# Optimization experiments

Measured on AMD Instinct MI355X. Metric: run time of the kernel, lower is better.

## Reference

```python
import jax, jax.numpy as jnp
import numpy as np

N_ENV = 100000
D_PS = 512
N_SPECIES = 4
N_SUPPORT = 256
N_STRUCT = 1000
ZETA = 2


def setup_inputs() -> dict:
    key = jax.random.key(0)
    k1, k2, k3, k4, k5 = jax.random.split(key, 5)
    power_spectrum = jax.random.normal(k1, (N_ENV, D_PS), dtype=jnp.float32)
    sp = jax.random.normal(k2, (N_SPECIES, N_SUPPORT, D_PS), dtype=jnp.float32)
    # CosineKernel asserts support points are unit-norm
    support_points = sp / jnp.linalg.norm(sp, axis=-1, keepdims=True)
    weights = jax.random.normal(k3, (N_SPECIES, 1, N_SUPPORT), dtype=jnp.float32)
    all_species = jax.random.randint(k4, (N_ENV,), 0, N_SPECIES, dtype=jnp.int64)
    structure_ids = jnp.sort(jax.random.randint(k5, (N_ENV,), 0, N_STRUCT, dtype=jnp.int64))
    return {
        "power_spectrum": power_spectrum,
        "support_points": support_points,
        "weights": weights,
        "all_species": all_species,
        "structure_ids": structure_ids,
    }


def reference(power_spectrum, support_points, weights, all_species, structure_ids):
    # Normalize each environment's power spectrum (CosineKernel)
    ps = power_spectrum / jnp.linalg.norm(power_spectrum, axis=1, keepdims=True)
    # Kernel of every environment against every species' support set: [N, S, M]
    k = jnp.einsum("nd,smd->nsm", ps, support_points) ** ZETA
    # Per-row energy contribution for each species: k @ weights[s].T -> [N, S]
    contrib = jnp.einsum("nsm,sm->ns", k, weights[:, 0, :])
    # Species masking: each row only contributes through its own species' kernel
    onehot = jax.nn.one_hot(all_species, N_SPECIES, dtype=contrib.dtype)  # [N, S]
    per_row = jnp.sum(contrib * onehot, axis=1)  # [N]
    # Segmented sum over structures (equivalent to looping over structures_slices)
    energy = jax.ops.segment_sum(per_row, structure_ids, num_segments=N_STRUCT)
    return energy[:, None]  # [n_structures, 1]
```

## Files before the change

kernel.cpp:

```cpp
#include <hip/hip_runtime.h>
#include <hip/hip_bf16.h>


constexpr int kNEnv     = 100000;
constexpr int kDPS      = 512;
constexpr int kNSpecies = 4;
constexpr int kNSupport = 256;
constexpr int kCap      = 32768;

constexpr int BN = 64;
constexpr int BK = 32;

typedef __attribute__((ext_vector_type(8))) short short8;
typedef __attribute__((ext_vector_type(4))) float f32x4;

__device__ __forceinline__ short8 pack_bf16x8(const float4& a, const float4& b) {
  union { short8 v; __hip_bfloat162 h[4]; } u;
  u.h[0] = __float22bfloat162_rn({a.x, a.y});
  u.h[1] = __float22bfloat162_rn({a.z, a.w});
  u.h[2] = __float22bfloat162_rn({b.x, b.y});
  u.h[3] = __float22bfloat162_rn({b.z, b.w});
  return u.v;
}

__global__ void scatter_convert_kernel(const float* __restrict__ sp,
                                       const int* __restrict__ species,
                                       const int* __restrict__ sid,
                                       int* __restrict__ cnt, int* __restrict__ perm,
                                       int* __restrict__ sidp, short* __restrict__ spb) {
  const int t = threadIdx.x;
  const int b = blockIdx.x;
  if (b < (kNSpecies * kNSupport * kDPS) / (256 * 8)) {
    const int base = (b * 256 + t) * 8;
    const float4 lo = *(const float4*)(sp + base);
    const float4 hi = *(const float4*)(sp + base + 4);
    *(short8*)(spb + base) = pack_bf16x8(lo, hi);
  }
  const int wv   = t >> 6;
  const int lane = t & 63;
  const int i    = b * 256 + t;
  const bool v   = i < kNEnv;
  int s = -1, g = 0;
  if (v) { s = species[i]; g = sid[i]; }

  unsigned long long m[kNSpecies];
  #pragma unroll
  for (int k = 0; k < kNSpecies; ++k) m[k] = __ballot(s == k);
  int r = 0;
  if (v) r = __popcll(m[s] & ((1ull << lane) - 1ull));

  __shared__ int wcnt[4][kNSpecies];
  __shared__ int wbase[4][kNSpecies];
  if (lane < kNSpecies) wcnt[wv][lane] = (int)__popcll(m[lane]);
  __syncthreads();
  if (t < kNSpecies) {
    const int k = t;
    const int tot = wcnt[0][k] + wcnt[1][k] + wcnt[2][k] + wcnt[3][k];
    int p = tot ? atomicAdd(&cnt[k], tot) : 0;
    #pragma unroll
    for (int wvi = 0; wvi < 4; ++wvi) { wbase[wvi][k] = p; p += wcnt[wvi][k]; }
  }
  __syncthreads();
  if (v) {
    const int d = s * kCap + wbase[wv][s] + r;
    perm[d] = i;
    sidp[d] = g;
  }
}

__global__ __launch_bounds__(256, 3) void gap_gemm_v8(
    const float* __restrict__ ps, const short* __restrict__ spb,
    const float* __restrict__ w, const int* __restrict__ cnt,
    const int* __restrict__ perm, const int* __restrict__ sidp,
    float* __restrict__ energy) {
  const int s     = blockIdx.z;
  const int count = min(cnt[s], kCap);
  const int tile0 = blockIdx.x * BN;
  if (tile0 >= count) return;

  __shared__ short a_lds[4][BN][32];
  __shared__ float red[4][BN];
  __shared__ float sqs[BN];

  const int tid  = threadIdx.x;
  const int wv   = tid >> 6;
  const int lane = tid & 63;
  const int l15  = lane & 15;
  const int lq   = lane >> 4;

  const int r0 = wv * 16 + (lane >> 2);
  const int q  = lane & 3;
  int ge = tile0 + r0;
  ge = ge < count ? ge : count - 1;
  const float* asrc = ps + (size_t)perm[s * kCap + ge] * kDPS + q * 8;

  const short* bptr[4];
  float wgt[4];
  const float* w_s = w + s * kNSupport;
  #pragma unroll
  for (int fj = 0; fj < 4; ++fj) {
    const int m = wv * 64 + fj * 16 + l15;
    bptr[fj] = spb + ((size_t)s * kNSupport + m) * kDPS + lq * 8;
    wgt[fj]  = w_s[m];
  }

  f32x4 acc[4][4];
  #pragma unroll
  for (int fi = 0; fi < 4; ++fi)
    #pragma unroll
    for (int fj = 0; fj < 4; ++fj) acc[fi][fj] = (f32x4)0.f;
  float sq = 0.f;

  float4 R[8];
  short8 bf0[4], bf1[4];

#define GLOAD8(G) do {                                                    \
    _Pragma("unroll")                                                     \
    for (int u = 0; u < 8; ++u)                                           \
      R[u] = *(const float4*)(asrc + (G) * 128 + (u >> 1) * 32 + (u & 1) * 4); \
  } while (0)

#define AWRITE8() do {                                                    \
    _Pragma("unroll")                                                     \
    for (int j = 0; j < 4; ++j) {                                         \
      const float4 va = R[2 * j], vb = R[2 * j + 1];                      \
      sq += va.x * va.x + va.y * va.y + va.z * va.z + va.w * va.w         \
          + vb.x * vb.x + vb.y * vb.y + vb.z * vb.z + vb.w * vb.w;        \
      *(short8*)&a_lds[j][r0][q * 8] = pack_bf16x8(va, vb);               \
    }                                                                     \
  } while (0)

#define BLOAD8(T, BF) do {                                                \
    _Pragma("unroll")                                                     \
    for (int fj = 0; fj < 4; ++fj)                                        \
      BF[fj] = *(const short8*)(bptr[fj] + (T) * BK);                     \
  } while (0)

#define ASTEP8(J, BF) do {                                                \
    short8 af[4];                                                         \
    _Pragma("unroll")                                                     \
    for (int fi = 0; fi < 4; ++fi)                                        \
      af[fi] = *(const short8*)&a_lds[J][fi * 16 + l15][lq * 8];          \
    __builtin_amdgcn_s_setprio(1);                                        \
    _Pragma("unroll")                                                     \
    for (int fi = 0; fi < 4; ++fi)                                        \
      _Pragma("unroll")                                                   \
      for (int fj = 0; fj < 4; ++fj)                                      \
        acc[fi][fj] = __builtin_amdgcn_mfma_f32_16x16x32_bf16(            \
            af[fi], BF[fj], acc[fi][fj], 0, 0, 0);                        \
    __builtin_amdgcn_s_setprio(0);                                        \
  } while (0)

#define GROUP8(G) do {                                                    \
    __builtin_amdgcn_s_barrier();              \
    AWRITE8();                                                            \
    asm volatile("s_waitcnt lgkmcnt(0)" ::: "memory");                    \
    __builtin_amdgcn_s_barrier();                     \
    __builtin_amdgcn_sched_barrier(0);                                    \
    if ((G) < 3) GLOAD8((G) + 1);             \
    __builtin_amdgcn_sched_barrier(0);                                    \
    BLOAD8((G) * 4 + 1, bf1); ASTEP8(0, bf0);                             \
    BLOAD8((G) * 4 + 2, bf0); ASTEP8(1, bf1);                             \
    BLOAD8((G) * 4 + 3, bf1); ASTEP8(2, bf0);                             \
    if ((G) < 3) BLOAD8((G) * 4 + 4, bf0);                                \
    ASTEP8(3, bf1);                                                       \
  } while (0)

  GLOAD8(0);
  BLOAD8(0, bf0);
  GROUP8(0);
  GROUP8(1);
  GROUP8(2);
  GROUP8(3);

#undef GROUP8
#undef ASTEP8
#undef BLOAD8
#undef AWRITE8
#undef GLOAD8

  sq += __shfl_xor(sq, 1, 64);
  sq += __shfl_xor(sq, 2, 64);
  if (q == 0) sqs[r0] = sq;

  #pragma unroll
  for (int fi = 0; fi < 4; ++fi) {
    #pragma unroll
    for (int r = 0; r < 4; ++r) {
      float p = 0.f;
      #pragma unroll
      for (int fj = 0; fj < 4; ++fj) {
        const float c = acc[fi][fj][r];
        p += c * c * wgt[fj];
      }
      p += __shfl_xor(p, 1, 64);
      p += __shfl_xor(p, 2, 64);
      p += __shfl_xor(p, 4, 64);
      p += __shfl_xor(p, 8, 64);
      if (l15 == 0) red[wv][fi * 16 + lq * 4 + r] = p;
    }
  }
  __syncthreads();
  if (tid < BN) {
    const float v = red[0][tid] + red[1][tid] + red[2][tid] + red[3][tid];
    const int g  = tile0 + tid;
    if (g < count) atomicAdd(&energy[sidp[s * kCap + g]], v / sqs[tid]);
  }
}

extern "C" void kernel_launch(void* const* d_in, const int* in_sizes, int n_in,
                              void* d_out, int out_size, void* d_ws, size_t ws_size,
                              hipStream_t stream) {
  const float* ps      = (const float*)d_in[0];
  const float* sp      = (const float*)d_in[1];
  const float* w       = (const float*)d_in[2];
  const int*   species = (const int*)d_in[3];
  const int*   sid     = (const int*)d_in[4];
  float* energy = (float*)d_out;

  char* wsb = (char*)d_ws;
  constexpr size_t kOffPerm = 256;
  constexpr size_t kOffSidp = kOffPerm + (size_t)kNSpecies * kCap * 4;
  constexpr size_t kOffSpb  = kOffSidp + (size_t)kNSpecies * kCap * 4;

  int*   cnt  = (int*)wsb;
  int*   perm = (int*)(wsb + kOffPerm);
  int*   sidp = (int*)(wsb + kOffSidp);
  short* spb  = (short*)(wsb + kOffSpb);

  hipMemsetAsync(cnt, 0, 16, stream);
  hipMemsetAsync(energy, 0, out_size * sizeof(float), stream);

  scatter_convert_kernel<<<(kNEnv + 255) / 256, 256, 0, stream>>>(
      sp, species, sid, cnt, perm, sidp, spb);

  dim3 grid(kCap / BN, 1, kNSpecies);
  gap_gemm_v8<<<grid, 256, 0, stream>>>(ps, spb, w, cnt, perm, sidp, energy);
}
```

Before: 337.6 us.

## Pre-tile bf16 support points for coalesced B loads and widen A-row gathers

The conversion kernel now writes the bf16 support points in a fragment-tiled layout, so each wave's MFMA B operand for a k-step is one contiguous 512-element block and the loads coalesce. The A gather is reorganised so each half-wave reads one full 512-byte contiguous row chunk, with per-row squared norms kept in eight partial sums and reduced by shuffles. All 16 B fragments for a group are loaded up front instead of being double-buffered per step. The launch-bounds occupancy hint of 3 is dropped. Holding 16 B fragments raises register pressure and may lower occupancy.

```diff
diff --git a/kernel.cpp b/kernel.cpp
--- a/kernel.cpp
+++ b/kernel.cpp
@@ -9,9 +9,9 @@
 constexpr int kCap      = 32768;
 
 constexpr int BN = 64;
-constexpr int BK = 32;
 
 typedef __attribute__((ext_vector_type(8))) short short8;
+typedef __attribute__((ext_vector_type(4))) short short4v;
 typedef __attribute__((ext_vector_type(4))) float f32x4;
 
 __device__ __forceinline__ short8 pack_bf16x8(const float4& a, const float4& b) {
@@ -23,18 +23,31 @@
   return u.v;
 }
 
+__device__ __forceinline__ short4v pack_bf16x4(const float4& a) {
+  union { short4v v; __hip_bfloat162 h[2]; } u;
+  u.h[0] = __float22bfloat162_rn({a.x, a.y});
+  u.h[1] = __float22bfloat162_rn({a.z, a.w});
+  return u.v;
+}
+
 __global__ void scatter_convert_kernel(const float* __restrict__ sp,
                                        const int* __restrict__ species,
                                        const int* __restrict__ sid,
                                        int* __restrict__ cnt, int* __restrict__ perm,
-                                       int* __restrict__ sidp, short* __restrict__ spb) {
+                                       int* __restrict__ sidp, short* __restrict__ spb2) {
   const int t = threadIdx.x;
   const int b = blockIdx.x;
   if (b < (kNSpecies * kNSupport * kDPS) / (256 * 8)) {
     const int base = (b * 256 + t) * 8;
     const float4 lo = *(const float4*)(sp + base);
     const float4 hi = *(const float4*)(sp + base + 4);
-    *(short8*)(spb + base) = pack_bf16x8(lo, hi);
+    const int s  = base >> 17;
+    const int m  = (base >> 9) & 255;
+    const int k  = base & 511;
+    const int j  = k >> 3;
+    const int tt = j >> 2, lqv = j & 3;
+    const int slot = (((s * 16 + tt) * 16 + (m >> 4)) * 16 + (m & 15)) * 4 + lqv;
+    *(short8*)(spb2 + (size_t)slot * 8) = pack_bf16x8(lo, hi);
   }
   const int wv   = t >> 6;
   const int lane = t & 63;
@@ -68,8 +81,8 @@
   }
 }
 
-__global__ __launch_bounds__(256, 3) void gap_gemm_v8(
-    const float* __restrict__ ps, const short* __restrict__ spb,
+__global__ __launch_bounds__(256) void gap_gemm_v9(
+    const float* __restrict__ ps, const short* __restrict__ spb2,
     const float* __restrict__ w, const int* __restrict__ cnt,
     const int* __restrict__ perm, const int* __restrict__ sidp,
     float* __restrict__ energy) {
@@ -87,21 +100,27 @@
   const int lane = tid & 63;
   const int l15  = lane & 15;
   const int lq   = lane >> 4;
-
-  const int r0 = wv * 16 + (lane >> 2);
-  const int q  = lane & 3;
-  int ge = tile0 + r0;
-  ge = ge < count ? ge : count - 1;
-  const float* asrc = ps + (size_t)perm[s * kCap + ge] * kDPS + q * 8;
+  const int lh   = lane >> 5;
+  const int l31  = lane & 31;
+
+  const char* psb = (const char*)ps;
+  unsigned int offs[8];
+  #pragma unroll
+  for (int u = 0; u < 8; ++u) {
+    int ge = tile0 + wv * 16 + 2 * u + lh;
+    ge = ge < count ? ge : count - 1;
+    offs[u] = (unsigned int)perm[s * kCap + ge] * 2048u + (unsigned int)l31 * 16u;
+  }
+  const int awb0 = ((l31 >> 3) * 64 * 32 + (wv * 16 + lh) * 32 + (l31 & 7) * 4) * 2;
 
   const short* bptr[4];
   float wgt[4];
   const float* w_s = w + s * kNSupport;
   #pragma unroll
   for (int fj = 0; fj < 4; ++fj) {
-    const int m = wv * 64 + fj * 16 + l15;
-    bptr[fj] = spb + ((size_t)s * kNSupport + m) * kDPS + lq * 8;
-    wgt[fj]  = w_s[m];
+    bptr[fj] = spb2 + ((size_t)(s * 16 + 0) * 16 + (wv * 4 + fj)) * 512
+             + (l15 * 4 + lq) * 8;
+    wgt[fj] = w_s[wv * 64 + fj * 16 + l15];
   }
 
   f32x4 acc[4][4];
@@ -109,34 +128,35 @@
   for (int fi = 0; fi < 4; ++fi)
     #pragma unroll
     for (int fj = 0; fj < 4; ++fj) acc[fi][fj] = (f32x4)0.f;
-  float sq = 0.f;
+  float sq8[8] = {0.f, 0.f, 0.f, 0.f, 0.f, 0.f, 0.f, 0.f};
 
   float4 R[8];
-  short8 bf0[4], bf1[4];
-
-#define GLOAD8(G) do {                                                    \
+  short8 bfs[16];
+
+#define GLOAD9(G) do {                                                    \
     _Pragma("unroll")                                                     \
     for (int u = 0; u < 8; ++u)                                           \
-      R[u] = *(const float4*)(asrc + (G) * 128 + (u >> 1) * 32 + (u & 1) * 4); \
-  } while (0)
-
-#define AWRITE8() do {                                                    \
-    _Pragma("unroll")                                                     \
-    for (int j = 0; j < 4; ++j) {                                         \
-      const float4 va = R[2 * j], vb = R[2 * j + 1];                      \
-      sq += va.x * va.x + va.y * va.y + va.z * va.z + va.w * va.w         \
-          + vb.x * vb.x + vb.y * vb.y + vb.z * vb.z + vb.w * vb.w;        \
-      *(short8*)&a_lds[j][r0][q * 8] = pack_bf16x8(va, vb);               \
+      R[u] = *(const float4*)(psb + offs[u] + (G) * 512);                 \
+  } while (0)
+
+#define AWRITE9() do {                                                    \
+    _Pragma("unroll")                                                     \
+    for (int u = 0; u < 8; ++u) {                                         \
+      const float4 va = R[u];                                             \
+      sq8[u] += va.x * va.x + va.y * va.y + va.z * va.z + va.w * va.w;    \
+      *(short4v*)((char*)&a_lds[0][0][0] + awb0 + u * 128) = pack_bf16x4(va); \
     }                                                                     \
   } while (0)
 
-#define BLOAD8(T, BF) do {                                                \
-    _Pragma("unroll")                                                     \
-    for (int fj = 0; fj < 4; ++fj)                                        \
-      BF[fj] = *(const short8*)(bptr[fj] + (T) * BK);                     \
-  } while (0)
-
-#define ASTEP8(J, BF) do {                                                \
+#define BLOADALL9(G) do {                                                 \
+    _Pragma("unroll")                                                     \
+    for (int st = 0; st < 4; ++st)                                        \
+      _Pragma("unroll")                                                   \
+      for (int fj = 0; fj < 4; ++fj)                                      \
+        bfs[st * 4 + fj] = *(const short8*)(bptr[fj] + ((G) * 4 + st) * 8192); \
+  } while (0)
+
+#define ASTEP9(J) do {                                                    \
     short8 af[4];                                                         \
     _Pragma("unroll")                                                     \
     for (int fi = 0; fi < 4; ++fi)                                        \
@@ -147,41 +167,45 @@
       _Pragma("unroll")                                                   \
       for (int fj = 0; fj < 4; ++fj)                                      \
         acc[fi][fj] = __builtin_amdgcn_mfma_f32_16x16x32_bf16(            \
-            af[fi], BF[fj], acc[fi][fj], 0, 0, 0);                        \
+            af[fi], bfs[(J) * 4 + fj], acc[fi][fj], 0, 0, 0);             \
     __builtin_amdgcn_s_setprio(0);                                        \
   } while (0)
 
-#define GROUP8(G) do {                                                    \
+#define GROUP9(G) do {                                                    \
     __builtin_amdgcn_s_barrier();              \
-    AWRITE8();                                                            \
+    AWRITE9();                                                            \
     asm volatile("s_waitcnt lgkmcnt(0)" ::: "memory");                    \
     __builtin_amdgcn_s_barrier();                     \
     __builtin_amdgcn_sched_barrier(0);                                    \
-    if ((G) < 3) GLOAD8((G) + 1);             \
+    BLOADALL9(G);                                                         \
     __builtin_amdgcn_sched_barrier(0);                                    \
-    BLOAD8((G) * 4 + 1, bf1); ASTEP8(0, bf0);                             \
-    BLOAD8((G) * 4 + 2, bf0); ASTEP8(1, bf1);                             \
-    BLOAD8((G) * 4 + 3, bf1); ASTEP8(2, bf0);                             \
-    if ((G) < 3) BLOAD8((G) * 4 + 4, bf0);                                \
-    ASTEP8(3, bf1);                                                       \
-  } while (0)
-
-  GLOAD8(0);
-  BLOAD8(0, bf0);
-  GROUP8(0);
-  GROUP8(1);
-  GROUP8(2);
-  GROUP8(3);
-
-#undef GROUP8
-#undef ASTEP8
-#undef BLOAD8
-#undef AWRITE8
-#undef GLOAD8
-
-  sq += __shfl_xor(sq, 1, 64);
-  sq += __shfl_xor(sq, 2, 64);
-  if (q == 0) sqs[r0] = sq;
+    if ((G) < 3) GLOAD9((G) + 1);                                         \
+    __builtin_amdgcn_sched_barrier(0);                                    \
+    ASTEP9(0); ASTEP9(1); ASTEP9(2); ASTEP9(3);                           \
+  } while (0)
+
+  GLOAD9(0);
+  GROUP9(0);
+  GROUP9(1);
+  GROUP9(2);
+  GROUP9(3);
+
+#undef GROUP9
+#undef ASTEP9
+#undef BLOADALL9
+#undef AWRITE9
+#undef GLOAD9
+
+  #pragma unroll
+  for (int u = 0; u < 8; ++u) {
+    float v = sq8[u];
+    v += __shfl_xor(v, 1, 64);
+    v += __shfl_xor(v, 2, 64);
+    v += __shfl_xor(v, 4, 64);
+    v += __shfl_xor(v, 8, 64);
+    v += __shfl_xor(v, 16, 64);
+    if (l31 == 0) sqs[wv * 16 + 2 * u + lh] = v;
+  }
 
   #pragma unroll
   for (int fi = 0; fi < 4; ++fi) {
@@ -226,14 +250,14 @@
   int*   cnt  = (int*)wsb;
   int*   perm = (int*)(wsb + kOffPerm);
   int*   sidp = (int*)(wsb + kOffSidp);
-  short* spb  = (short*)(wsb + kOffSpb);
+  short* spb2 = (short*)(wsb + kOffSpb);
 
   hipMemsetAsync(cnt, 0, 16, stream);
   hipMemsetAsync(energy, 0, out_size * sizeof(float), stream);
 
   scatter_convert_kernel<<<(kNEnv + 255) / 256, 256, 0, stream>>>(
-      sp, species, sid, cnt, perm, sidp, spb);
+      sp, species, sid, cnt, perm, sidp, spb2);
 
   dim3 grid(kCap / BN, 1, kNSpecies);
-  gap_gemm_v8<<<grid, 256, 0, stream>>>(ps, spb, w, cnt, perm, sidp, energy);
-}
+  gap_gemm_v9<<<grid, 256, 0, stream>>>(ps, spb2, w, cnt, perm, sidp, energy);
+}
```

After: 358.3 us. 1.06x slower.
